# Kernel optimization log

Measured on AMD Instinct MI355X. Metric: run time of the kernel, lower is better.

The kernel has to match this reference:

```python
import jax, jax.numpy as jnp
import numpy as np

B, S, D, H, DH = 4, 2048, 512, 8, 64  # batch, seq, input_dim, heads, per-head output_dim


def setup_inputs() -> dict:
    key = jax.random.key(0)
    ks = jax.random.split(key, 10)
    scale = 0.02
    inp = {
        "x": jax.random.normal(ks[0], (B, S, D), dtype=jnp.float32),
        "biological_mask": jnp.ones((B, S), dtype=bool),
        "Wq": jax.random.normal(ks[1], (D, H * DH), dtype=jnp.float32) * scale,
        "bq": jnp.zeros((H * DH,), dtype=jnp.float32),
        "Wk": jax.random.normal(ks[2], (D, H * DH), dtype=jnp.float32) * scale,
        "bk": jnp.zeros((H * DH,), dtype=jnp.float32),
        "Wv": jax.random.normal(ks[3], (D, H * DH), dtype=jnp.float32) * scale,
        "bv": jnp.zeros((H * DH,), dtype=jnp.float32),
        "Wo": jax.random.normal(ks[4], (H * DH, DH), dtype=jnp.float32) * scale,
        "bo": jnp.zeros((DH,), dtype=jnp.float32),
        "prior_weight": jnp.full((1,), 0.1, dtype=jnp.float32),
    }
    return inp


def reference(x, biological_mask, Wq, bq, Wk, bk, Wv, bv, Wo, bo, prior_weight):
    b, s, _ = x.shape
    inv_sqrt_dh = jnp.float32(1.0 / np.sqrt(DH))
    # projections -> [B,H,S,DH]
    q = (x @ Wq + bq).reshape(b, s, H, DH).transpose(0, 2, 1, 3)
    k = (x @ Wk + bk).reshape(b, s, H, DH).transpose(0, 2, 1, 3)
    v = (x @ Wv + bv).reshape(b, s, H, DH).transpose(0, 2, 1, 3)
    # scores [B,H,S,S]
    scores = jnp.einsum("bhqd,bhkd->bhqk", q, k) * inv_sqrt_dh
    # biological prior: identity matrix, broadcast over batch and heads
    prior = jnp.eye(s, dtype=scores.dtype)[None, None, :, :]
    scores = scores + prior_weight[0] * prior
    attn = jax.nn.softmax(scores, axis=-1)  # dropout is identity in eval mode
    attended = jnp.einsum("bhqk,bhkd->bhqd", attn, v)
    attended = attended.transpose(0, 2, 1, 3).reshape(b, s, H * DH)
    return attended @ Wo + bo
```

## Files before the change

### kernel.cpp

```cpp
#include <hip/hip_runtime.h>
#include <hip/hip_bf16.h>

#define B_ 4
#define S_ 2048
#define D_ 512
#define H_ 8
#define DH_ 64
#define HD_ 512
#define M_ 8192
#define QKVN 1536
#define QKN 1024
#define LOG2E 1.4426950408889634f

typedef __attribute__((ext_vector_type(8))) short bf16x8;
typedef __attribute__((ext_vector_type(4))) float f32x4;
typedef unsigned short u16;

__device__ inline u16 f2bf(float f) {
    __hip_bfloat16 h = __float2bfloat16(f);
    return *reinterpret_cast<u16*>(&h);
}

__device__ inline void async_cp16(const void* g, void* l) {
    __builtin_amdgcn_global_load_lds(
        (const __attribute__((address_space(1))) unsigned int*)g,
        (__attribute__((address_space(3))) unsigned int*)l, 16, 0, 0);
}

__global__ __launch_bounds__(256) void castbf(const float* __restrict__ src,
                                              u16* __restrict__ dst, int n8)
{
    int i = blockIdx.x * 256 + threadIdx.x;
    if (i < n8) {
        float4 a = *reinterpret_cast<const float4*>(&src[(size_t)i * 8]);
        float4 b = *reinterpret_cast<const float4*>(&src[(size_t)i * 8 + 4]);
        bf16x8 o;
        o[0] = f2bf(a.x); o[1] = f2bf(a.y); o[2] = f2bf(a.z); o[3] = f2bf(a.w);
        o[4] = f2bf(b.x); o[5] = f2bf(b.y); o[6] = f2bf(b.z); o[7] = f2bf(b.w);
        *reinterpret_cast<bf16x8*>(&dst[(size_t)i * 8]) = o;
    }
}

__global__ __launch_bounds__(256) void wprep(
    const float* __restrict__ Wq, const float* __restrict__ Wk,
    const float* __restrict__ Wv, const float* __restrict__ Wo,
    u16* __restrict__ WqkvT, u16* __restrict__ WoT)
{
    const int z = blockIdx.z;
    const float* src; u16* dst; int R, C;
    if (z < 3) { src = (z == 0) ? Wq : (z == 1) ? Wk : Wv;
                 dst = WqkvT + (size_t)z * 512 * 512; R = 512; C = 512; }
    else       { if (blockIdx.x) return; src = Wo; dst = WoT; R = 512; C = 64; }

    __shared__ u16 T[64][65];
    const int tid = threadIdx.x;
    const int c0 = blockIdx.x * 64, r0 = blockIdx.y * 64;
#pragma unroll
    for (int i = 0; i < 4; ++i) {
        int idx = i * 256 + tid;
        int r = idx >> 4, q4 = (idx & 15) << 2;
        float4 vv = *reinterpret_cast<const float4*>(&src[(size_t)(r0 + r) * C + c0 + q4]);
        T[r][q4 + 0] = f2bf(vv.x); T[r][q4 + 1] = f2bf(vv.y);
        T[r][q4 + 2] = f2bf(vv.z); T[r][q4 + 3] = f2bf(vv.w);
    }
    __syncthreads();
#pragma unroll
    for (int i = 0; i < 2; ++i) {
        int idx = i * 256 + tid;
        int cc = idx >> 3, jj = idx & 7;
        bf16x8 o;
#pragma unroll
        for (int e = 0; e < 8; ++e) o[e] = (short)T[jj * 8 + e][cc];
        *reinterpret_cast<bf16x8*>(&dst[(size_t)(c0 + cc) * R + r0 + jj * 8]) = o;
    }
}

__global__ __launch_bounds__(256) void gemm_qkv(
    const u16* __restrict__ A, const u16* __restrict__ BT,
    const float* __restrict__ bq, const float* __restrict__ bk,
    const float* __restrict__ bv, u16* __restrict__ qk,
    u16* __restrict__ vT, float qscale)
{
    __shared__ __align__(16) u16 As[128 * 64];
    __shared__ __align__(16) u16 Bs[128 * 64];
    const int tid = threadIdx.x, lane = tid & 63, w = tid >> 6;
    const int l15 = lane & 15, l4 = lane >> 4;
    const int tm = blockIdx.y * 128, tn = blockIdx.x * 128;
    const int wm = (w >> 1) * 64, wn = (w & 1) * 64;

    f32x4 acc[4][4] = {};

    for (int k0 = 0; k0 < 512; k0 += 64) {
#pragma unroll
        for (int i = 0; i < 4; ++i) {
            int call = w * 4 + i;
            int c = call * 64 + lane;
            int r = c >> 3, j = c & 7;
            async_cp16(A + (size_t)(tm + r) * 512 + k0 + ((j ^ (r & 7)) << 3),
                       &As[call * 512]);
            async_cp16(BT + (size_t)(tn + r) * 512 + k0 + ((j ^ (r & 7)) << 3),
                       &Bs[call * 512]);
        }
        __syncthreads();
#pragma unroll
        for (int ks = 0; ks < 2; ++ks) {
            bf16x8 af[4], bf[4];
#pragma unroll
            for (int mf = 0; mf < 4; ++mf) {
                int r = wm + mf * 16 + l15;
                int j = ks * 4 + l4;
                af[mf] = *reinterpret_cast<const bf16x8*>(&As[(r * 8 + (j ^ (r & 7))) * 8]);
            }
#pragma unroll
            for (int nf = 0; nf < 4; ++nf) {
                int r = wn + nf * 16 + l15;
                int j = ks * 4 + l4;
                bf[nf] = *reinterpret_cast<const bf16x8*>(&Bs[(r * 8 + (j ^ (r & 7))) * 8]);
            }
#pragma unroll
            for (int mf = 0; mf < 4; ++mf)
#pragma unroll
                for (int nf = 0; nf < 4; ++nf)
                    acc[mf][nf] = __builtin_amdgcn_mfma_f32_16x16x32_bf16(
                        af[mf], bf[nf], acc[mf][nf], 0, 0, 0);
        }
        __syncthreads();
    }
#pragma unroll
    for (int nf = 0; nf < 4; ++nf) {
        const int col = tn + wn + nf * 16 + l15;
        if (col < QKN) {
            const float bias_v = (col < 512) ? bq[col] : bk[col - 512];
            const float scl = (col < 512) ? qscale : 1.0f;
#pragma unroll
            for (int mf = 0; mf < 4; ++mf)
#pragma unroll
                for (int r = 0; r < 4; ++r) {
                    int row = tm + wm + mf * 16 + l4 * 4 + r;
                    qk[(size_t)row * QKN + col] = f2bf((acc[mf][nf][r] + bias_v) * scl);
                }
        } else {
            const int dcol = col - QKN;
            const float bias_v = bv[dcol];
            const int hh = dcol >> 6, dd = dcol & 63;
#pragma unroll
            for (int mf = 0; mf < 4; ++mf) {
                int row0 = tm + wm + mf * 16 + l4 * 4;
                int bb = row0 >> 11, s0 = row0 & 2047;
                ushort4 pk;
                pk.x = f2bf(acc[mf][nf][0] + bias_v);
                pk.y = f2bf(acc[mf][nf][1] + bias_v);
                pk.z = f2bf(acc[mf][nf][2] + bias_v);
                pk.w = f2bf(acc[mf][nf][3] + bias_v);
                *reinterpret_cast<ushort4*>(
                    &vT[((size_t)(bb * 8 + hh) * 64 + dd) * S_ + s0]) = pk;
            }
        }
    }
}

__global__ __launch_bounds__(256, 4) void flash_mfma(
    const u16* __restrict__ qk, const u16* __restrict__ vT,
    const float* __restrict__ pw_ptr, u16* __restrict__ att)
{
    __shared__ __align__(16) u16 Kb[2][4096];
    __shared__ __align__(16) u16 Vb[2][4096];

    const int tid = threadIdx.x, lane = tid & 63, w = tid >> 6;
    const int l15 = lane & 15, l4 = lane >> 4;
    const int bid = blockIdx.x;
    const int x = bid & 7, g = bid >> 3;
    const int bh = x * 4 + (g >> 5), qt = g & 31;
    const int h = bh & 7, b = bh >> 3;
    const float pwl = pw_ptr[0] * LOG2E;

    const u16* qbase = qk + (size_t)b * S_ * QKN + h * 64;
    const u16* kbase = qbase + 512;
    const u16* vtb   = vT + (size_t)bh * DH_ * S_;

    const int qrow0 = qt * 64 + w * 16;
    bf16x8 qb[2];
#pragma unroll
    for (int ks2 = 0; ks2 < 2; ++ks2)
        qb[ks2] = *reinterpret_cast<const bf16x8*>(
            &qbase[(size_t)(qrow0 + l15) * QKN + ks2 * 32 + l4 * 8]);

    f32x4 accv[4] = {};
    float l_r = 0.f;
    const int diag_t = qt;

#define STAGE(buf, jj) do {                                                        \
    _Pragma("unroll")                                                              \
    for (int i_ = 0; i_ < 2; ++i_) {                                               \
        int call_ = w * 2 + i_;                                                    \
        int c_ = call_ * 64 + lane;                                                \
        int rho_ = c_ >> 3, j_ = c_ & 7;                                           \
        int pi_ = (rho_ & 32) | ((rho_ & 12) << 1) | ((rho_ & 16) >> 2)            \
                | (rho_ & 3);                                                      \
        async_cp16(kbase + (size_t)((jj) + pi_) * QKN + ((j_ ^ (rho_ & 7)) << 3),  \
                   &Kb[buf][call_ * 512]);                                         \
        async_cp16(vtb + (size_t)rho_ * S_ + (jj) + ((j_ ^ (rho_ & 7)) << 3),      \
                   &Vb[buf][call_ * 512]);                                         \
    } } while (0)

    STAGE(0, 0);
    __syncthreads();
    int cur = 0;

    for (int t = 0; t < 32; ++t) {
        const int j0 = t << 6;
        if (t < 31) STAGE(cur ^ 1, j0 + 64);

        f32x4 s[4] = {};
        __builtin_amdgcn_s_setprio(1);
#pragma unroll
        for (int c = 0; c < 4; ++c)
#pragma unroll
            for (int ks2 = 0; ks2 < 2; ++ks2) {
                const int rr = c * 16 + l15;
                const int sl = ks2 * 4 + l4;
                bf16x8 ka = *reinterpret_cast<const bf16x8*>(
                    &Kb[cur][(rr * 8 + (sl ^ (rr & 7))) * 8]);
                s[c] = __builtin_amdgcn_mfma_f32_16x16x32_bf16(ka, qb[ks2], s[c], 0, 0, 0);
            }
        __builtin_amdgcn_s_setprio(0);

        if (t == diag_t) {
#pragma unroll
            for (int c = 0; c < 4; ++c)
#pragma unroll
                for (int r = 0; r < 4; ++r) {
                    int kv = (c >> 1) * 32 + l4 * 8 + (c & 1) * 4 + r;
                    if (j0 + kv == qrow0 + l15) s[c][r] += pwl;
                }
        }

        bf16x8 pa[2];
#pragma unroll
        for (int ks = 0; ks < 2; ++ks)
#pragma unroll
            for (int d2 = 0; d2 < 2; ++d2)
#pragma unroll
                for (int r = 0; r < 4; ++r) {
                    float p = exp2f(s[ks * 2 + d2][r]);
                    l_r += p;
                    pa[ks][d2 * 4 + r] = (short)f2bf(p);
                }

        __builtin_amdgcn_s_setprio(1);
#pragma unroll
        for (int nf = 0; nf < 4; ++nf) {
            const int d = nf * 16 + l15;
#pragma unroll
            for (int ks = 0; ks < 2; ++ks) {
                const int sl = ks * 4 + l4;
                bf16x8 vb = *reinterpret_cast<const bf16x8*>(
                    &Vb[cur][(d * 8 + (sl ^ (d & 7))) * 8]);
                accv[nf] = __builtin_amdgcn_mfma_f32_16x16x32_bf16(pa[ks], vb, accv[nf], 0, 0, 0);
            }
        }
        __builtin_amdgcn_s_setprio(0);

        __syncthreads();
        cur ^= 1;
    }
#undef STAGE

    float lt = l_r;
    lt += __shfl_xor(lt, 16);
    lt += __shfl_xor(lt, 32);
#pragma unroll
    for (int r = 0; r < 4; ++r) {
        float inv = 1.0f / __shfl(lt, l4 * 4 + r);
        int row = qrow0 + l4 * 4 + r;
#pragma unroll
        for (int nf = 0; nf < 4; ++nf)
            att[(size_t)(b * S_ + row) * HD_ + h * 64 + nf * 16 + l15] =
                f2bf(accv[nf][r] * inv);
    }
}

__global__ __launch_bounds__(64) void out_proj(
    const u16* __restrict__ att, const u16* __restrict__ WoT,
    const float* __restrict__ bo, float* __restrict__ out)
{
    const int lane = threadIdx.x;
    const int l15 = lane & 15, l4 = lane >> 4;
    const int row0 = blockIdx.x * 16;

    f32x4 acc[4] = {};
#pragma unroll 4
    for (int ks = 0; ks < 16; ++ks) {
        bf16x8 a = *reinterpret_cast<const bf16x8*>(
            &att[(size_t)(row0 + l15) * 512 + ks * 32 + l4 * 8]);
#pragma unroll
        for (int nf = 0; nf < 4; ++nf) {
            bf16x8 bb = *reinterpret_cast<const bf16x8*>(
                &WoT[(size_t)(nf * 16 + l15) * 512 + ks * 32 + l4 * 8]);
            acc[nf] = __builtin_amdgcn_mfma_f32_16x16x32_bf16(a, bb, acc[nf], 0, 0, 0);
        }
    }
#pragma unroll
    for (int nf = 0; nf < 4; ++nf) {
        int n = nf * 16 + l15;
        float bias_v = bo[n];
#pragma unroll
        for (int r = 0; r < 4; ++r)
            out[(size_t)(row0 + l4 * 4 + r) * 64 + n] = acc[nf][r] + bias_v;
    }
}

extern "C" void kernel_launch(void* const* d_in, const int* in_sizes, int n_in,
                              void* d_out, int out_size, void* d_ws, size_t ws_size,
                              hipStream_t stream)
{
    const float* x  = (const float*)d_in[0];
    const float* Wq = (const float*)d_in[2];
    const float* bq = (const float*)d_in[3];
    const float* Wk = (const float*)d_in[4];
    const float* bk = (const float*)d_in[5];
    const float* Wv = (const float*)d_in[6];
    const float* bv = (const float*)d_in[7];
    const float* Wo = (const float*)d_in[8];
    const float* bo = (const float*)d_in[9];
    const float* pw = (const float*)d_in[10];

    u16* ws = (u16*)d_ws;
    size_t o = 0;
    u16* xb    = ws + o; o += (size_t)M_ * D_;
    u16* WqkvT = ws + o; o += (size_t)QKVN * D_;
    u16* WoT   = ws + o; o += (size_t)DH_ * HD_;
    u16* qkb   = ws + o; o += (size_t)M_ * QKN;
    u16* vTt   = ws + o; o += (size_t)M_ * HD_;
    u16* att   = ws + o; o += (size_t)M_ * HD_;

    dim3 blk(256);
    castbf<<<dim3(M_ * D_ / 8 / 256), blk, 0, stream>>>(x, xb, M_ * D_ / 8);
    wprep<<<dim3(8, 8, 4), blk, 0, stream>>>(Wq, Wk, Wv, Wo, WqkvT, WoT);

    gemm_qkv<<<dim3(QKVN / 128, M_ / 128), blk, 0, stream>>>(
        xb, WqkvT, bq, bk, bv, qkb, vTt, 0.125f * LOG2E);

    flash_mfma<<<dim3(1024), blk, 0, stream>>>(qkb, vTt, pw, att);

    out_proj<<<dim3(M_ / 16), dim3(64), 0, stream>>>(att, WoT, bo, (float*)d_out);
}
```

Baseline: 107.9 us.

## Merge prep kernels, compute softmax row sums via MFMA, precompute LDS offsets

Merges the x cast and weight transpose kernels into a single launch, which removes one kernel launch. In the flash kernel the softmax denominator is now accumulated by an MFMA against a ones vector instead of scalar adds plus cross-lane shuffles. The swizzled LDS offsets for K and V are computed once outside the loop, and the occupancy hint is dropped from launch bounds. The extra MFMA and the precomputed offsets raise register use. Because the denominator now sums the bf16-rounded probabilities, it matches what the PV product uses.

```diff
diff --git a/kernel.cpp b/kernel.cpp
--- a/kernel.cpp
+++ b/kernel.cpp
@@ -27,33 +27,37 @@
         (__attribute__((address_space(3))) unsigned int*)l, 16, 0, 0);
 }
 
-__global__ __launch_bounds__(256) void castbf(const float* __restrict__ src,
-                                              u16* __restrict__ dst, int n8)
-{
-    int i = blockIdx.x * 256 + threadIdx.x;
-    if (i < n8) {
-        float4 a = *reinterpret_cast<const float4*>(&src[(size_t)i * 8]);
-        float4 b = *reinterpret_cast<const float4*>(&src[(size_t)i * 8 + 4]);
-        bf16x8 o;
-        o[0] = f2bf(a.x); o[1] = f2bf(a.y); o[2] = f2bf(a.z); o[3] = f2bf(a.w);
-        o[4] = f2bf(b.x); o[5] = f2bf(b.y); o[6] = f2bf(b.z); o[7] = f2bf(b.w);
-        *reinterpret_cast<bf16x8*>(&dst[(size_t)i * 8]) = o;
-    }
-}
-
-__global__ __launch_bounds__(256) void wprep(
-    const float* __restrict__ Wq, const float* __restrict__ Wk,
-    const float* __restrict__ Wv, const float* __restrict__ Wo,
+__global__ __launch_bounds__(256) void prep_all(
+    const float* __restrict__ x, const float* __restrict__ Wq,
+    const float* __restrict__ Wk, const float* __restrict__ Wv,
+    const float* __restrict__ Wo, u16* __restrict__ xb,
     u16* __restrict__ WqkvT, u16* __restrict__ WoT)
 {
     const int z = blockIdx.z;
+    const int tid = threadIdx.x;
+
+    if (z == 4) {
+        const int id = blockIdx.y * 64 + blockIdx.x;
+#pragma unroll
+        for (int it = 0; it < 4; ++it) {
+            int i = it * 131072 + id * 256 + tid;
+            float4 a = *reinterpret_cast<const float4*>(&x[(size_t)i * 8]);
+            float4 b = *reinterpret_cast<const float4*>(&x[(size_t)i * 8 + 4]);
+            bf16x8 o;
+            o[0] = f2bf(a.x); o[1] = f2bf(a.y); o[2] = f2bf(a.z); o[3] = f2bf(a.w);
+            o[4] = f2bf(b.x); o[5] = f2bf(b.y); o[6] = f2bf(b.z); o[7] = f2bf(b.w);
+            *reinterpret_cast<bf16x8*>(&xb[(size_t)i * 8]) = o;
+        }
+        return;
+    }
+
     const float* src; u16* dst; int R, C;
-    if (z < 3) { src = (z == 0) ? Wq : (z == 1) ? Wk : Wv;
+    if (z < 3) { if (blockIdx.x >= 8) return;
+                 src = (z == 0) ? Wq : (z == 1) ? Wk : Wv;
                  dst = WqkvT + (size_t)z * 512 * 512; R = 512; C = 512; }
     else       { if (blockIdx.x) return; src = Wo; dst = WoT; R = 512; C = 64; }
 
     __shared__ u16 T[64][65];
-    const int tid = threadIdx.x;
     const int c0 = blockIdx.x * 64, r0 = blockIdx.y * 64;
 #pragma unroll
     for (int i = 0; i < 4; ++i) {
@@ -159,7 +163,7 @@
     }
 }
 
-__global__ __launch_bounds__(256, 4) void flash_mfma(
+__global__ __launch_bounds__(256) void flash_mfma(
     const u16* __restrict__ qk, const u16* __restrict__ vT,
     const float* __restrict__ pw_ptr, u16* __restrict__ att)
 {
@@ -181,12 +185,27 @@
     const int qrow0 = qt * 64 + w * 16;
     bf16x8 qb[2];
 #pragma unroll
-    for (int ks2 = 0; ks2 < 2; ++ks2)
-        qb[ks2] = *reinterpret_cast<const bf16x8*>(
-            &qbase[(size_t)(qrow0 + l15) * QKN + ks2 * 32 + l4 * 8]);
+    for (int ks = 0; ks < 2; ++ks)
+        qb[ks] = *reinterpret_cast<const bf16x8*>(
+            &qbase[(size_t)(qrow0 + l15) * QKN + ks * 32 + l4 * 8]);
+
+    const bf16x8 ones = {(short)0x3F80, (short)0x3F80, (short)0x3F80, (short)0x3F80,
+                         (short)0x3F80, (short)0x3F80, (short)0x3F80, (short)0x3F80};
+
+    int koffs[4][2], voffs[4][2];
+#pragma unroll
+    for (int c = 0; c < 4; ++c)
+#pragma unroll
+        for (int ks = 0; ks < 2; ++ks) {
+            const int rr = c * 16 + l15;
+            const int sl = ks * 4 + l4;
+            koffs[c][ks] = (rr * 8 + (sl ^ (rr & 7))) * 8;
+            const int d = c * 16 + l15;
+            voffs[c][ks] = (d * 8 + (sl ^ (d & 7))) * 8;
+        }
 
     f32x4 accv[4] = {};
-    float l_r = 0.f;
+    f32x4 accl = {};
     const int diag_t = qt;
 
 #define STAGE(buf, jj) do {                                                        \
@@ -211,17 +230,17 @@
         const int j0 = t << 6;
         if (t < 31) STAGE(cur ^ 1, j0 + 64);
 
+        const u16* kbuf = &Kb[cur][0];
+        const u16* vbuf = &Vb[cur][0];
+
         f32x4 s[4] = {};
         __builtin_amdgcn_s_setprio(1);
 #pragma unroll
         for (int c = 0; c < 4; ++c)
 #pragma unroll
-            for (int ks2 = 0; ks2 < 2; ++ks2) {
-                const int rr = c * 16 + l15;
-                const int sl = ks2 * 4 + l4;
-                bf16x8 ka = *reinterpret_cast<const bf16x8*>(
-                    &Kb[cur][(rr * 8 + (sl ^ (rr & 7))) * 8]);
-                s[c] = __builtin_amdgcn_mfma_f32_16x16x32_bf16(ka, qb[ks2], s[c], 0, 0, 0);
+            for (int ks = 0; ks < 2; ++ks) {
+                bf16x8 ka = *reinterpret_cast<const bf16x8*>(kbuf + koffs[c][ks]);
+                s[c] = __builtin_amdgcn_mfma_f32_16x16x32_bf16(ka, qb[ks], s[c], 0, 0, 0);
             }
         __builtin_amdgcn_s_setprio(0);
 
@@ -241,24 +260,19 @@
 #pragma unroll
             for (int d2 = 0; d2 < 2; ++d2)
 #pragma unroll
-                for (int r = 0; r < 4; ++r) {
-                    float p = exp2f(s[ks * 2 + d2][r]);
-                    l_r += p;
-                    pa[ks][d2 * 4 + r] = (short)f2bf(p);
-                }
+                for (int r = 0; r < 4; ++r)
+                    pa[ks][d2 * 4 + r] = (short)f2bf(exp2f(s[ks * 2 + d2][r]));
 
         __builtin_amdgcn_s_setprio(1);
-#pragma unroll
-        for (int nf = 0; nf < 4; ++nf) {
-            const int d = nf * 16 + l15;
+        accl = __builtin_amdgcn_mfma_f32_16x16x32_bf16(pa[0], ones, accl, 0, 0, 0);
+        accl = __builtin_amdgcn_mfma_f32_16x16x32_bf16(pa[1], ones, accl, 0, 0, 0);
+#pragma unroll
+        for (int nf = 0; nf < 4; ++nf)
 #pragma unroll
             for (int ks = 0; ks < 2; ++ks) {
-                const int sl = ks * 4 + l4;
-                bf16x8 vb = *reinterpret_cast<const bf16x8*>(
-                    &Vb[cur][(d * 8 + (sl ^ (d & 7))) * 8]);
+                bf16x8 vb = *reinterpret_cast<const bf16x8*>(vbuf + voffs[nf][ks]);
                 accv[nf] = __builtin_amdgcn_mfma_f32_16x16x32_bf16(pa[ks], vb, accv[nf], 0, 0, 0);
             }
-        }
         __builtin_amdgcn_s_setprio(0);
 
         __syncthreads();
@@ -266,12 +280,9 @@
     }
 #undef STAGE
 
-    float lt = l_r;
-    lt += __shfl_xor(lt, 16);
-    lt += __shfl_xor(lt, 32);
 #pragma unroll
     for (int r = 0; r < 4; ++r) {
-        float inv = 1.0f / __shfl(lt, l4 * 4 + r);
+        float inv = 1.0f / accl[r];
         int row = qrow0 + l4 * 4 + r;
 #pragma unroll
         for (int nf = 0; nf < 4; ++nf)
@@ -335,8 +346,7 @@
     u16* att   = ws + o; o += (size_t)M_ * HD_;
 
     dim3 blk(256);
-    castbf<<<dim3(M_ * D_ / 8 / 256), blk, 0, stream>>>(x, xb, M_ * D_ / 8);
-    wprep<<<dim3(8, 8, 4), blk, 0, stream>>>(Wq, Wk, Wv, Wo, WqkvT, WoT);
+    prep_all<<<dim3(64, 8, 5), blk, 0, stream>>>(x, Wq, Wk, Wv, Wo, xb, WqkvT, WoT);
 
     gemm_qkv<<<dim3(QKVN / 128, M_ / 128), blk, 0, stream>>>(
         xb, WqkvT, bq, bk, bv, qkb, vTt, 0.125f * LOG2E);
```

Measured after the change: 112.5 us. 4.3% more time.
